# Kernel optimization log

Hardware: AMD Instinct MI355X
Metric: run time of the kernel (lower is better)

## Reference

```python
import jax, jax.numpy as jnp
import numpy as np

H, C = 8, 32          # heads, per-head channels (h_feats)
NEG_SLOPE = 0.2


def setup_inputs() -> dict:
    key = jax.random.key(0)
    ks = jax.random.split(key, 9)
    N, E, F_IN, F_E = 50000, 800000, 128, 16
    x = jax.random.normal(ks[0], (N, F_IN), jnp.float32)
    edge_index = jax.random.randint(ks[1], (2, E), 0, N, jnp.int64)
    edge_attr = jax.random.normal(ks[2], (E, F_E), jnp.float32)
    s = 1.0 / np.sqrt(F_IN)
    W = jax.random.normal(ks[3], (H * C, F_IN), jnp.float32) * s
    W_edge = jax.random.normal(ks[4], (H * C, F_E), jnp.float32) * (1.0 / np.sqrt(F_E))
    att_src = jax.random.normal(ks[5], (H, C), jnp.float32) * (1.0 / np.sqrt(C))
    att_dst = jax.random.normal(ks[6], (H, C), jnp.float32) * (1.0 / np.sqrt(C))
    att_edge = jax.random.normal(ks[7], (H, C), jnp.float32) * (1.0 / np.sqrt(C))
    bias = jnp.zeros((C,), jnp.float32)
    return {"x": x, "edge_index": edge_index, "edge_attr": edge_attr,
            "W": W, "W_edge": W_edge, "att_src": att_src, "att_dst": att_dst,
            "att_edge": att_edge, "bias": bias}


def reference(x, edge_index, edge_attr, W, W_edge, att_src, att_dst, att_edge, bias):
    N = x.shape[0]
    src, dst = edge_index[0], edge_index[1]

    # --- add self loops, edge_attr fill_value='mean' (per-dst mean of incoming attrs) ---
    deg = jax.ops.segment_sum(jnp.ones_like(dst, dtype=edge_attr.dtype), dst, num_segments=N)
    loop_attr = jax.ops.segment_sum(edge_attr, dst, num_segments=N) / jnp.maximum(deg, 1.0)[:, None]
    loop = jnp.arange(N, dtype=src.dtype)
    src = jnp.concatenate([src, loop])
    dst = jnp.concatenate([dst, loop])
    ea = jnp.concatenate([edge_attr, loop_attr], axis=0)  # [E+N, F_e]

    # --- node projection and per-node attention terms ---
    xh = (x @ W.T).reshape(N, H, C)                      # [N,H,C]
    a_src = jnp.einsum('nhc,hc->nh', xh, att_src)        # [N,H]
    a_dst = jnp.einsum('nhc,hc->nh', xh, att_dst)        # [N,H]

    # edge attention folded: (lin_edge(e).view(E,H,C) * att_edge).sum(-1) == e @ M
    M = jnp.einsum('hcf,hc->fh', W_edge.reshape(H, C, -1), att_edge)  # [F_e,H]
    a_edge = ea @ M                                      # [E+N,H]

    alpha = a_src[src] + a_dst[dst] + a_edge             # [E+N,H]
    alpha = jnp.where(alpha >= 0, alpha, NEG_SLOPE * alpha)

    # --- scatter-softmax over edges grouped by dst node ---
    amax = jax.ops.segment_max(alpha, dst, num_segments=N)  # every node has a self loop
    ex = jnp.exp(alpha - amax[dst])
    denom = jax.ops.segment_sum(ex, dst, num_segments=N)
    att = ex / denom[dst]                                # [E+N,H]

    # --- weighted message scatter-sum ---
    msg = xh[src] * att[..., None]                       # [E+N,H,C]
    out = jax.ops.segment_sum(msg, dst, num_segments=N)  # [N,H,C]
    return out.mean(axis=1) + bias                       # concat=False -> head mean
```

## Files before the change

kernel.cpp:

```cpp
#include <hip/hip_runtime.h>
#include <hip/hip_fp16.h>
#include <math.h>

#define H 8
#define C 32
#define HC 256
#define FE 16
#define FIN 128
#define NEG_SLOPE 0.2f

typedef __attribute__((ext_vector_type(8))) short bf16x8;
typedef __attribute__((ext_vector_type(4))) float f32x4;

__device__ __forceinline__ unsigned short f2bf(float f) {
  unsigned int u = __float_as_uint(f);
  unsigned int lsb = (u >> 16) & 1u;
  u += 0x7fffu + lsb;
  return (unsigned short)(u >> 16);
}
__device__ __forceinline__ float bf2f(unsigned short s) {
  return __uint_as_float(((unsigned int)s) << 16);
}
__device__ __forceinline__ unsigned short f2h(float f) {
  return __half_as_ushort(__float2half(f));
}
__device__ __forceinline__ float h2f(unsigned short s) {
  return __half2float(__ushort_as_half(s));
}

__device__ __forceinline__ void split8(const float* v, bf16x8& hi, bf16x8& lo) {
#pragma unroll
  for (int i = 0; i < 8; ++i) {
    unsigned int u = __float_as_uint(v[i]);
    unsigned int hu = u & 0xffff0000u;
    float r = v[i] - __uint_as_float(hu);
    hi[i] = (short)(hu >> 16);
    lo[i] = (short)f2bf(r);
  }
}

__global__ __launch_bounds__(256) void k_xh(const float* __restrict__ x,
                                            const unsigned short* __restrict__ Whi,
                                            const unsigned short* __restrict__ Wlo,
                                            const float* __restrict__ att_src,
                                            const float* __restrict__ att_dst,
                                            unsigned short* __restrict__ xhb,
                                            float* __restrict__ a_src,
                                            float* __restrict__ a_dst,
                                            unsigned short* __restrict__ a_srch, int N) {
  int t = threadIdx.x;
  int w = t >> 6, lane = t & 63;
  int n15 = lane & 15, q = lane >> 4;
  int nodeBase = blockIdx.x * 128 + w * 32;
  int chBase = blockIdx.y * 128;

  f32x4 acc[8][2];
#pragma unroll
  for (int mt = 0; mt < 8; ++mt)
#pragma unroll
    for (int nt = 0; nt < 2; ++nt) acc[mt][nt] = (f32x4)(0.f);

  for (int ks = 0; ks < 4; ++ks) {
    int kOff = ks * 32 + q * 8;
    bf16x8 Bhi[2], Blo[2];
#pragma unroll
    for (int nt = 0; nt < 2; ++nt) {
      int node = nodeBase + nt * 16 + n15;
      int rn = (node < N) ? node : (N - 1);
      const float* px = &x[(size_t)rn * FIN + kOff];
      float vb[8];
      *(float4*)&vb[0] = *(const float4*)px;
      *(float4*)&vb[4] = *(const float4*)(px + 4);
      split8(vb, Bhi[nt], Blo[nt]);
    }
#pragma unroll
    for (int mt = 0; mt < 8; ++mt) {
      int widx = ((chBase + mt * 16 + n15) << 7) + kOff;
      bf16x8 Ahi = *(const bf16x8*)&Whi[widx];
      bf16x8 Alo = *(const bf16x8*)&Wlo[widx];
#pragma unroll
      for (int nt = 0; nt < 2; ++nt) {
        acc[mt][nt] = __builtin_amdgcn_mfma_f32_16x16x32_bf16(Ahi, Bhi[nt], acc[mt][nt], 0, 0, 0);
        acc[mt][nt] = __builtin_amdgcn_mfma_f32_16x16x32_bf16(Ahi, Blo[nt], acc[mt][nt], 0, 0, 0);
        acc[mt][nt] = __builtin_amdgcn_mfma_f32_16x16x32_bf16(Alo, Bhi[nt], acc[mt][nt], 0, 0, 0);
      }
    }
  }

  float ps[2][4] = {{0.f,0.f,0.f,0.f},{0.f,0.f,0.f,0.f}};
  float pd[2][4] = {{0.f,0.f,0.f,0.f},{0.f,0.f,0.f,0.f}};
#pragma unroll
  for (int mt = 0; mt < 8; ++mt) {
    int hl = mt >> 1;
#pragma unroll
    for (int r = 0; r < 4; ++r) {
      int ch = chBase + mt * 16 + q * 4 + r;
      float as_c = att_src[ch], ad_c = att_dst[ch];
#pragma unroll
      for (int nt = 0; nt < 2; ++nt) {
        float val = acc[mt][nt][r];
        ps[nt][hl] = fmaf(val, as_c, ps[nt][hl]);
        pd[nt][hl] = fmaf(val, ad_c, pd[nt][hl]);
      }
    }
#pragma unroll
    for (int nt = 0; nt < 2; ++nt) {
      int node = nodeBase + nt * 16 + n15;
      if (node < N) {
        ushort4 us;
        us.x = f2bf(acc[mt][nt][0]); us.y = f2bf(acc[mt][nt][1]);
        us.z = f2bf(acc[mt][nt][2]); us.w = f2bf(acc[mt][nt][3]);
        *(ushort4*)&xhb[(size_t)node * HC + chBase + mt * 16 + q * 4] = us;
      }
    }
  }
#pragma unroll
  for (int nt = 0; nt < 2; ++nt)
#pragma unroll
    for (int hl = 0; hl < 4; ++hl) {
      ps[nt][hl] += __shfl_xor(ps[nt][hl], 16, 64);
      ps[nt][hl] += __shfl_xor(ps[nt][hl], 32, 64);
      pd[nt][hl] += __shfl_xor(pd[nt][hl], 16, 64);
      pd[nt][hl] += __shfl_xor(pd[nt][hl], 32, 64);
    }
  if (q == 0) {
#pragma unroll
    for (int nt = 0; nt < 2; ++nt) {
      int node = nodeBase + nt * 16 + n15;
      if (node < N) {
        *(float4*)&a_src[node * H + blockIdx.y * 4] = make_float4(ps[nt][0], ps[nt][1], ps[nt][2], ps[nt][3]);
        *(float4*)&a_dst[node * H + blockIdx.y * 4] = make_float4(pd[nt][0], pd[nt][1], pd[nt][2], pd[nt][3]);
        unsigned int p0 = (unsigned int)f2h(ps[nt][0]) | ((unsigned int)f2h(ps[nt][1]) << 16);
        unsigned int p1 = (unsigned int)f2h(ps[nt][2]) | ((unsigned int)f2h(ps[nt][3]) << 16);
        *(uint2*)&a_srch[(size_t)node * H + blockIdx.y * 4] = make_uint2(p0, p1);
      }
    }
  }
}

__global__ __launch_bounds__(256) void k_deg(const int* __restrict__ ei,
                                             int* __restrict__ deg,
                                             int* __restrict__ rank,
                                             const float* __restrict__ W,
                                             unsigned short* __restrict__ Whi,
                                             unsigned short* __restrict__ Wlo, int E) {
  int e = blockIdx.x * 256 + threadIdx.x;
  if (e < HC * FIN) {
    float v = W[e];
    unsigned int u = __float_as_uint(v);
    unsigned int hu = u & 0xffff0000u;
    Whi[e] = (unsigned short)(hu >> 16);
    Wlo[e] = f2bf(v - __uint_as_float(hu));
  }
  if (e < E) rank[e] = atomicAdd(&deg[ei[E + e]], 1);
}

__global__ __launch_bounds__(256) void k_scan1(const int* __restrict__ deg,
                                               int* __restrict__ bsum, int N) {
  int t = threadIdx.x;
  int i = blockIdx.x * 256 + t;
  int v = (i < N) ? deg[i] : 0;
#pragma unroll
  for (int m = 1; m < 64; m <<= 1) v += __shfl_xor(v, m, 64);
  __shared__ int wsum[4];
  if ((t & 63) == 0) wsum[t >> 6] = v;
  __syncthreads();
  if (t == 0) bsum[blockIdx.x] = wsum[0] + wsum[1] + wsum[2] + wsum[3];
}

__global__ __launch_bounds__(256) void k_scan23(const int* __restrict__ deg,
                                                const int* __restrict__ bsum,
                                                int* __restrict__ rowptr, int N, int E, int nb) {
  __shared__ int sb[256];
  __shared__ int buf[256];
  int t = threadIdx.x;
  sb[t] = (t < nb) ? bsum[t] : 0;
  int i = blockIdx.x * 256 + t;
  int v = (i < N) ? deg[i] : 0;
  buf[t] = v;
  __syncthreads();
  for (int off = 1; off < 256; off <<= 1) {
    int y1 = (t >= off) ? sb[t - off] : 0;
    int y2 = (t >= off) ? buf[t - off] : 0;
    __syncthreads();
    sb[t] += y1;
    buf[t] += y2;
    __syncthreads();
  }
  int bofs = (blockIdx.x == 0) ? 0 : sb[blockIdx.x - 1];
  if (i < N) rowptr[i] = bofs + buf[t] - v;
  if (i == 0) rowptr[N] = E;
}

__global__ __launch_bounds__(256) void k_edge_scatter(const int* __restrict__ ei,
                                                      const float* __restrict__ ea,
                                                      const float* __restrict__ W_edge,
                                                      const float* __restrict__ att_edge,
                                                      const unsigned short* __restrict__ a_srch,
                                                      const int* __restrict__ rowptr,
                                                      const int* __restrict__ rank,
                                                      unsigned int* __restrict__ recs,
                                                      int* __restrict__ sarr, int E) {
  __shared__ float Ms[FE * H];
  int t = threadIdx.x;
  if (t < FE * H) {
    int f = t >> 3, h = t & 7;
    float acc = 0.f;
#pragma unroll
    for (int c = 0; c < C; ++c)
      acc += W_edge[(h * C + c) * FE + f] * att_edge[h * C + c];
    Ms[f * H + h] = acc;
  }
  __syncthreads();
  int e0 = blockIdx.x * 512 + t;
  int e1 = e0 + 256;
  bool va = (e0 < E), vb = (e1 < E);
  int ca = va ? e0 : 0, cb = vb ? e1 : 0;
  int s0 = ei[ca], d0 = ei[E + ca];
  int s1 = ei[cb], d1 = ei[E + cb];
  const float4* pA = (const float4*)&ea[(size_t)ca * FE];
  const float4* pB = (const float4*)&ea[(size_t)cb * FE];
  float4 A0 = pA[0], A1 = pA[1], A2 = pA[2], A3 = pA[3];
  float4 B0 = pB[0], B1 = pB[1], B2 = pB[2], B3 = pB[3];
  int rk0 = rank[ca], rk1 = rank[cb];
  int rp0 = rowptr[d0], rp1 = rowptr[d1];
  uint4 asA = *(const uint4*)&a_srch[(size_t)s0 * H];
  uint4 asB = *(const uint4*)&a_srch[(size_t)s1 * H];

  float eavA[FE] = {A0.x, A0.y, A0.z, A0.w, A1.x, A1.y, A1.z, A1.w,
                    A2.x, A2.y, A2.z, A2.w, A3.x, A3.y, A3.z, A3.w};
  float eavB[FE] = {B0.x, B0.y, B0.z, B0.w, B1.x, B1.y, B1.z, B1.w,
                    B2.x, B2.y, B2.z, B2.w, B3.x, B3.y, B3.z, B3.w};
  float oA[H], oB[H];
#pragma unroll
  for (int h = 0; h < H; ++h) {
    float aa = 0.f, ab = 0.f;
#pragma unroll
    for (int f = 0; f < FE; ++f) {
      float m = Ms[f * H + h];
      aa += eavA[f] * m;
      ab += eavB[f] * m;
    }
    oA[h] = aa; oB[h] = ab;
  }
  unsigned int asw[2][4] = {{asA.x, asA.y, asA.z, asA.w}, {asB.x, asB.y, asB.z, asB.w}};
  if (va) {
    int pos = rp0 + rk0;
    unsigned int rec[H];
#pragma unroll
    for (int h = 0; h < H; ++h) {
      float asv = h2f((unsigned short)((h & 1) ? (asw[0][h >> 1] >> 16) : (asw[0][h >> 1] & 0xffffu)));
      rec[h] = (unsigned int)f2h(oA[h] + asv) | ((unsigned int)f2h(oA[h]) << 16);
    }
    uint4* rp = (uint4*)&recs[(size_t)pos * 8];
    rp[0] = make_uint4(rec[0], rec[1], rec[2], rec[3]);
    rp[1] = make_uint4(rec[4], rec[5], rec[6], rec[7]);
    sarr[pos] = s0;
  }
  if (vb) {
    int pos = rp1 + rk1;
    unsigned int rec[H];
#pragma unroll
    for (int h = 0; h < H; ++h) {
      float asv = h2f((unsigned short)((h & 1) ? (asw[1][h >> 1] >> 16) : (asw[1][h >> 1] & 0xffffu)));
      rec[h] = (unsigned int)f2h(oB[h] + asv) | ((unsigned int)f2h(oB[h]) << 16);
    }
    uint4* rp = (uint4*)&recs[(size_t)pos * 8];
    rp[0] = make_uint4(rec[0], rec[1], rec[2], rec[3]);
    rp[1] = make_uint4(rec[4], rec[5], rec[6], rec[7]);
    sarr[pos] = s1;
  }
}

__global__ __launch_bounds__(256) void k_node(const unsigned short* __restrict__ xhb,
                                              const float* __restrict__ a_src,
                                              const float* __restrict__ a_dst,
                                              const unsigned int* __restrict__ recs,
                                              const int* __restrict__ sarr,
                                              const int* __restrict__ rowptr,
                                              const float* __restrict__ bias,
                                              float* __restrict__ out, int N) {
  __shared__ float wlds[4][512];
  __shared__ int   slds[4][64];
  int wv = threadIdx.x >> 6;
  int lane = threadIdx.x & 63;
  int n = blockIdx.x * 4 + wv;
  if (n >= N) return;
  int start = rowptr[n];
  int deg = rowptr[n + 1] - start;
  int jmax = (deg < 64) ? deg : 64;
  int nit = (jmax + 7) >> 3;
  int padded = nit << 3;
  int h = lane & 7, esub = lane >> 3;
  float adst = a_dst[n * H + h];
  float asrc = a_src[n * H + h];

  if (lane < padded) slds[wv][lane] = (lane < jmax) ? sarr[start + lane] : n;

  const unsigned int* rb = recs + (size_t)start * 8 + lane;
  unsigned int u[8] = {0, 0, 0, 0, 0, 0, 0, 0};
#pragma unroll
  for (int it = 0; it < 8; ++it)
    if (it < nit) u[it] = rb[it * 64];

  float den = 0.f, psum = 0.f;
#pragma unroll
  for (int it = 0; it < 8; ++it)
    if (it < nit) {
      int j = it * 8 + esub;
      bool val = (j < jmax);
      float raw = h2f((unsigned short)(u[it] >> 16));
      float a = h2f((unsigned short)(u[it] & 0xffffu)) + adst;
      a = fmaxf(a, NEG_SLOPE * a);
      float w = val ? __expf(a) : 0.f;
      psum += val ? raw : 0.f;
      den += w;
      wlds[wv][it * 64 + lane] = w;
    }
  for (int j0 = 64; j0 < deg; j0 += 8) {
    int j = j0 + esub;
    if (j < deg) {
      unsigned int t = recs[(size_t)(start + j) * 8 + h];
      psum += h2f((unsigned short)(t >> 16));
      float a = h2f((unsigned short)(t & 0xffffu)) + adst;
      a = fmaxf(a, NEG_SLOPE * a);
      den += __expf(a);
    }
  }
#pragma unroll
  for (int m = 8; m <= 32; m <<= 1) {
    den += __shfl_xor(den, m, 64);
    psum += __shfl_xor(psum, m, 64);
  }
  float aself = asrc + adst + psum / fmaxf((float)deg, 1.f);
  aself = fmaxf(aself, NEG_SLOPE * aself);
  float wself = __expf(aself);
  float inv = 1.f / (den + wself);

  int hc = lane >> 3;
  float inv_c  = __shfl(inv, hc, 64);
  float ws_c   = __shfl(wself, hc, 64);
  float adst_c = __shfl(adst, hc, 64);
  float accx, accy, accz, accw;
  {
    uint2 su = ((const uint2*)(xhb + (((size_t)n) << 8)))[lane];
    accx = ws_c * __uint_as_float(su.x << 16);
    accy = ws_c * __uint_as_float(su.x & 0xffff0000u);
    accz = ws_c * __uint_as_float(su.y << 16);
    accw = ws_c * __uint_as_float(su.y & 0xffff0000u);
  }
  uint2 v0[8]; float w0[8];
  if (padded > 0) {
#pragma unroll
    for (int k = 0; k < 8; ++k) {
      w0[k] = wlds[wv][k * 8 + hc];
      v0[k] = ((const uint2*)(xhb + (((size_t)slds[wv][k]) << 8)))[lane];
    }
  }
  for (int j0 = 0; j0 < padded; j0 += 8) {
    uint2 v1[8]; float w1[8];
    int jn = j0 + 8;
    if (jn < padded) {
#pragma unroll
      for (int k = 0; k < 8; ++k) {
        w1[k] = wlds[wv][(jn + k) * 8 + hc];
        v1[k] = ((const uint2*)(xhb + (((size_t)slds[wv][jn + k]) << 8)))[lane];
      }
    }
#pragma unroll
    for (int k = 0; k < 8; ++k) {
      accx = fmaf(__uint_as_float(v0[k].x << 16), w0[k], accx);
      accy = fmaf(__uint_as_float(v0[k].x & 0xffff0000u), w0[k], accy);
      accz = fmaf(__uint_as_float(v0[k].y << 16), w0[k], accz);
      accw = fmaf(__uint_as_float(v0[k].y & 0xffff0000u), w0[k], accw);
    }
#pragma unroll
    for (int k = 0; k < 8; ++k) { v0[k] = v1[k]; w0[k] = w1[k]; }
  }
  for (int j = 64; j < deg; ++j) {
    unsigned int t = recs[(size_t)(start + j) * 8 + hc];
    int src = sarr[start + j];
    float a = h2f((unsigned short)(t & 0xffffu)) + adst_c;
    a = fmaxf(a, NEG_SLOPE * a);
    float wj = __expf(a);
    uint2 v = ((const uint2*)(xhb + (((size_t)src) << 8)))[lane];
    accx = fmaf(__uint_as_float(v.x << 16), wj, accx);
    accy = fmaf(__uint_as_float(v.x & 0xffff0000u), wj, accy);
    accz = fmaf(__uint_as_float(v.y << 16), wj, accz);
    accw = fmaf(__uint_as_float(v.y & 0xffff0000u), wj, accw);
  }
  accx *= inv_c; accy *= inv_c; accz *= inv_c; accw *= inv_c;

#pragma unroll
  for (int m = 8; m <= 32; m <<= 1) {
    accx += __shfl_xor(accx, m, 64);
    accy += __shfl_xor(accy, m, 64);
    accz += __shfl_xor(accz, m, 64);
    accw += __shfl_xor(accw, m, 64);
  }
  if (lane < 8) {
    float4 b = ((const float4*)bias)[lane];
    float4 o;
    o.x = accx * 0.125f + b.x;
    o.y = accy * 0.125f + b.y;
    o.z = accz * 0.125f + b.z;
    o.w = accw * 0.125f + b.w;
    ((float4*)&out[(size_t)n * C])[lane] = o;
  }
}

extern "C" void kernel_launch(void* const* d_in, const int* in_sizes, int n_in,
                              void* d_out, int out_size, void* d_ws, size_t ws_size,
                              hipStream_t stream) {
  const float* x        = (const float*)d_in[0];
  const int*   ei       = (const int*)d_in[1];
  const float* ea       = (const float*)d_in[2];
  const float* W        = (const float*)d_in[3];
  const float* W_edge   = (const float*)d_in[4];
  const float* att_src  = (const float*)d_in[5];
  const float* att_dst  = (const float*)d_in[6];
  const float* att_edge = (const float*)d_in[7];
  const float* bias     = (const float*)d_in[8];
  float* out = (float*)d_out;

  int N = in_sizes[0] / FIN;
  int E = in_sizes[1] / 2;
  int nb = (N + 255) / 256;

  char* ws = (char*)d_ws;
  auto take = [&](size_t bytes) {
    char* p = ws;
    ws += (bytes + 255) & ~(size_t)255;
    return p;
  };
  unsigned short* xhb    = (unsigned short*)take((size_t)N * HC * 2);
  float*          a_src  = (float*)take((size_t)N * H * 4);
  float*          a_dst  = (float*)take((size_t)N * H * 4);
  unsigned short* a_srch = (unsigned short*)take((size_t)N * H * 2);
  unsigned int*   recs   = (unsigned int*)take((size_t)E * 32);
  int*            sarr   = (int*)take((size_t)E * 4);
  unsigned short* Whi    = (unsigned short*)take((size_t)HC * FIN * 2);
  unsigned short* Wlo    = (unsigned short*)take((size_t)HC * FIN * 2);
  int*            deg    = (int*)take((size_t)N * 4);
  int*            rowptr = (int*)take((size_t)(N + 1) * 4);
  int*            rank   = (int*)take((size_t)E * 4);
  int*            bsum   = (int*)take((size_t)nb * 4);

  hipMemsetAsync(deg, 0, (size_t)N * 4, stream);
  k_deg<<<(E + 255) / 256, 256, 0, stream>>>(ei, deg, rank, W, Whi, Wlo, E);
  k_xh<<<dim3((N + 127) / 128, 2), 256, 0, stream>>>(x, Whi, Wlo, att_src, att_dst, xhb, a_src, a_dst, a_srch, N);
  k_scan1<<<nb, 256, 0, stream>>>(deg, bsum, N);
  k_scan23<<<nb, 256, 0, stream>>>(deg, bsum, rowptr, N, E, nb);
  k_edge_scatter<<<(E + 511) / 512, 256, 0, stream>>>(ei, ea, W_edge, att_edge, a_srch, rowptr, rank, recs, sarr, E);
  k_node<<<(N + 3) / 4, 256, 0, stream>>>(xhb, a_src, a_dst, recs, sarr, rowptr, bias, out, N);
}
```

Before: 303.4 us.

## Replace edge record scatter with permutation and compute edge attention in node kernel

The edge-scatter kernel, which computed per-edge attention logits and wrote 32-byte half-precision records plus source ids in CSR order, becomes a small kernel that writes only (src, edge id) pairs at each CSR position. The node kernel now gathers the edge attributes (64 bytes, in random original order), computes the edge attention term with the folded matrix held in shared memory, and adds the source term itself. This removes the record write and re-read but adds uncoalesced 64-byte gathers and extra math per edge in the node kernel. It also drops the software double buffering of the neighbour feature loads.

```diff
diff --git a/kernel.cpp b/kernel.cpp
--- a/kernel.cpp
+++ b/kernel.cpp
@@ -192,98 +192,49 @@
   if (i == 0) rowptr[N] = E;
 }
 
-__global__ __launch_bounds__(256) void k_edge_scatter(const int* __restrict__ ei,
-                                                      const float* __restrict__ ea,
-                                                      const float* __restrict__ W_edge,
-                                                      const float* __restrict__ att_edge,
-                                                      const unsigned short* __restrict__ a_srch,
-                                                      const int* __restrict__ rowptr,
-                                                      const int* __restrict__ rank,
-                                                      unsigned int* __restrict__ recs,
-                                                      int* __restrict__ sarr, int E) {
-  __shared__ float Ms[FE * H];
-  int t = threadIdx.x;
-  if (t < FE * H) {
-    int f = t >> 3, h = t & 7;
-    float acc = 0.f;
-#pragma unroll
-    for (int c = 0; c < C; ++c)
-      acc += W_edge[(h * C + c) * FE + f] * att_edge[h * C + c];
-    Ms[f * H + h] = acc;
-  }
-  __syncthreads();
-  int e0 = blockIdx.x * 512 + t;
+__global__ __launch_bounds__(256) void k_perm(const int* __restrict__ ei,
+                                              const int* __restrict__ rowptr,
+                                              const int* __restrict__ rank,
+                                              int2* __restrict__ pr, int E) {
+  int e0 = blockIdx.x * 512 + threadIdx.x;
   int e1 = e0 + 256;
   bool va = (e0 < E), vb = (e1 < E);
   int ca = va ? e0 : 0, cb = vb ? e1 : 0;
   int s0 = ei[ca], d0 = ei[E + ca];
   int s1 = ei[cb], d1 = ei[E + cb];
-  const float4* pA = (const float4*)&ea[(size_t)ca * FE];
-  const float4* pB = (const float4*)&ea[(size_t)cb * FE];
-  float4 A0 = pA[0], A1 = pA[1], A2 = pA[2], A3 = pA[3];
-  float4 B0 = pB[0], B1 = pB[1], B2 = pB[2], B3 = pB[3];
   int rk0 = rank[ca], rk1 = rank[cb];
   int rp0 = rowptr[d0], rp1 = rowptr[d1];
-  uint4 asA = *(const uint4*)&a_srch[(size_t)s0 * H];
-  uint4 asB = *(const uint4*)&a_srch[(size_t)s1 * H];
-
-  float eavA[FE] = {A0.x, A0.y, A0.z, A0.w, A1.x, A1.y, A1.z, A1.w,
-                    A2.x, A2.y, A2.z, A2.w, A3.x, A3.y, A3.z, A3.w};
-  float eavB[FE] = {B0.x, B0.y, B0.z, B0.w, B1.x, B1.y, B1.z, B1.w,
-                    B2.x, B2.y, B2.z, B2.w, B3.x, B3.y, B3.z, B3.w};
-  float oA[H], oB[H];
-#pragma unroll
-  for (int h = 0; h < H; ++h) {
-    float aa = 0.f, ab = 0.f;
-#pragma unroll
-    for (int f = 0; f < FE; ++f) {
-      float m = Ms[f * H + h];
-      aa += eavA[f] * m;
-      ab += eavB[f] * m;
-    }
-    oA[h] = aa; oB[h] = ab;
-  }
-  unsigned int asw[2][4] = {{asA.x, asA.y, asA.z, asA.w}, {asB.x, asB.y, asB.z, asB.w}};
-  if (va) {
-    int pos = rp0 + rk0;
-    unsigned int rec[H];
-#pragma unroll
-    for (int h = 0; h < H; ++h) {
-      float asv = h2f((unsigned short)((h & 1) ? (asw[0][h >> 1] >> 16) : (asw[0][h >> 1] & 0xffffu)));
-      rec[h] = (unsigned int)f2h(oA[h] + asv) | ((unsigned int)f2h(oA[h]) << 16);
-    }
-    uint4* rp = (uint4*)&recs[(size_t)pos * 8];
-    rp[0] = make_uint4(rec[0], rec[1], rec[2], rec[3]);
-    rp[1] = make_uint4(rec[4], rec[5], rec[6], rec[7]);
-    sarr[pos] = s0;
-  }
-  if (vb) {
-    int pos = rp1 + rk1;
-    unsigned int rec[H];
-#pragma unroll
-    for (int h = 0; h < H; ++h) {
-      float asv = h2f((unsigned short)((h & 1) ? (asw[1][h >> 1] >> 16) : (asw[1][h >> 1] & 0xffffu)));
-      rec[h] = (unsigned int)f2h(oB[h] + asv) | ((unsigned int)f2h(oB[h]) << 16);
-    }
-    uint4* rp = (uint4*)&recs[(size_t)pos * 8];
-    rp[0] = make_uint4(rec[0], rec[1], rec[2], rec[3]);
-    rp[1] = make_uint4(rec[4], rec[5], rec[6], rec[7]);
-    sarr[pos] = s1;
-  }
+  if (va) pr[rp0 + rk0] = make_int2(s0, ca);
+  if (vb) pr[rp1 + rk1] = make_int2(s1, cb);
 }
 
 __global__ __launch_bounds__(256) void k_node(const unsigned short* __restrict__ xhb,
                                               const float* __restrict__ a_src,
+                                              const unsigned short* __restrict__ a_srch,
                                               const float* __restrict__ a_dst,
-                                              const unsigned int* __restrict__ recs,
-                                              const int* __restrict__ sarr,
+                                              const float* __restrict__ ea,
+                                              const float* __restrict__ W_edge,
+                                              const float* __restrict__ att_edge,
+                                              const int2* __restrict__ pr,
                                               const int* __restrict__ rowptr,
                                               const float* __restrict__ bias,
                                               float* __restrict__ out, int N) {
+  __shared__ float Ms[FE * H];
   __shared__ float wlds[4][512];
   __shared__ int   slds[4][64];
-  int wv = threadIdx.x >> 6;
-  int lane = threadIdx.x & 63;
+  int t = threadIdx.x;
+  if (t < FE * H) {
+    int f = t >> 3, hh = t & 7;
+    float acc = 0.f;
+#pragma unroll
+    for (int c = 0; c < C; ++c)
+      acc += W_edge[(hh * C + c) * FE + f] * att_edge[hh * C + c];
+    Ms[f * H + hh] = acc;
+  }
+  __syncthreads();
+
+  int wv = t >> 6;
+  int lane = t & 63;
   int n = blockIdx.x * 4 + wv;
   if (n >= N) return;
   int start = rowptr[n];
@@ -295,13 +246,20 @@
   float adst = a_dst[n * H + h];
   float asrc = a_src[n * H + h];
 
-  if (lane < padded) slds[wv][lane] = (lane < jmax) ? sarr[start + lane] : n;
-
-  const unsigned int* rb = recs + (size_t)start * 8 + lane;
-  unsigned int u[8] = {0, 0, 0, 0, 0, 0, 0, 0};
-#pragma unroll
-  for (int it = 0; it < 8; ++it)
-    if (it < nit) u[it] = rb[it * 64];
+  int2 pe[8];
+#pragma unroll
+  for (int it = 0; it < 8; ++it) {
+    pe[it] = make_int2(n, 0);
+    if (it < nit) {
+      int j = it * 8 + esub;
+      if (j < jmax) pe[it] = pr[start + j];
+    }
+  }
+  if (h == 0) {
+#pragma unroll
+    for (int it = 0; it < 8; ++it)
+      if (it < nit) slds[wv][it * 8 + esub] = pe[it].x;
+  }
 
   float den = 0.f, psum = 0.f;
 #pragma unroll
@@ -309,21 +267,36 @@
     if (it < nit) {
       int j = it * 8 + esub;
       bool val = (j < jmax);
-      float raw = h2f((unsigned short)(u[it] >> 16));
-      float a = h2f((unsigned short)(u[it] & 0xffffu)) + adst;
+      const float4* pq = (const float4*)&ea[(size_t)pe[it].y * FE];
+      float4 q0 = pq[0], q1 = pq[1], q2 = pq[2], q3 = pq[3];
+      float ev[16] = {q0.x, q0.y, q0.z, q0.w, q1.x, q1.y, q1.z, q1.w,
+                      q2.x, q2.y, q2.z, q2.w, q3.x, q3.y, q3.z, q3.w};
+      float aev = 0.f;
+#pragma unroll
+      for (int f = 0; f < FE; ++f) aev = fmaf(ev[f], Ms[f * H + h], aev);
+      float asv = h2f(a_srch[(size_t)pe[it].x * H + h]);
+      float a = aev + asv + adst;
       a = fmaxf(a, NEG_SLOPE * a);
       float w = val ? __expf(a) : 0.f;
-      psum += val ? raw : 0.f;
+      psum += val ? aev : 0.f;
       den += w;
       wlds[wv][it * 64 + lane] = w;
     }
   for (int j0 = 64; j0 < deg; j0 += 8) {
     int j = j0 + esub;
     if (j < deg) {
-      unsigned int t = recs[(size_t)(start + j) * 8 + h];
-      psum += h2f((unsigned short)(t >> 16));
-      float a = h2f((unsigned short)(t & 0xffffu)) + adst;
+      int2 pe2 = pr[start + j];
+      const float4* pq = (const float4*)&ea[(size_t)pe2.y * FE];
+      float4 q0 = pq[0], q1 = pq[1], q2 = pq[2], q3 = pq[3];
+      float ev[16] = {q0.x, q0.y, q0.z, q0.w, q1.x, q1.y, q1.z, q1.w,
+                      q2.x, q2.y, q2.z, q2.w, q3.x, q3.y, q3.z, q3.w};
+      float aev = 0.f;
+#pragma unroll
+      for (int f = 0; f < FE; ++f) aev = fmaf(ev[f], Ms[f * H + h], aev);
+      float asv = h2f(a_srch[(size_t)pe2.x * H + h]);
+      float a = aev + asv + adst;
       a = fmaxf(a, NEG_SLOPE * a);
+      psum += aev;
       den += __expf(a);
     }
   }
@@ -349,41 +322,35 @@
     accz = ws_c * __uint_as_float(su.y << 16);
     accw = ws_c * __uint_as_float(su.y & 0xffff0000u);
   }
-  uint2 v0[8]; float w0[8];
-  if (padded > 0) {
+  for (int j0 = 0; j0 < padded; j0 += 8) {
+    uint2 v[8]; float wj[8];
 #pragma unroll
     for (int k = 0; k < 8; ++k) {
-      w0[k] = wlds[wv][k * 8 + hc];
-      v0[k] = ((const uint2*)(xhb + (((size_t)slds[wv][k]) << 8)))[lane];
-    }
-  }
-  for (int j0 = 0; j0 < padded; j0 += 8) {
-    uint2 v1[8]; float w1[8];
-    int jn = j0 + 8;
-    if (jn < padded) {
-#pragma unroll
-      for (int k = 0; k < 8; ++k) {
-        w1[k] = wlds[wv][(jn + k) * 8 + hc];
-        v1[k] = ((const uint2*)(xhb + (((size_t)slds[wv][jn + k]) << 8)))[lane];
-      }
+      wj[k] = wlds[wv][(j0 + k) * 8 + hc];
+      v[k] = ((const uint2*)(xhb + (((size_t)slds[wv][j0 + k]) << 8)))[lane];
     }
 #pragma unroll
     for (int k = 0; k < 8; ++k) {
-      accx = fmaf(__uint_as_float(v0[k].x << 16), w0[k], accx);
-      accy = fmaf(__uint_as_float(v0[k].x & 0xffff0000u), w0[k], accy);
-      accz = fmaf(__uint_as_float(v0[k].y << 16), w0[k], accz);
-      accw = fmaf(__uint_as_float(v0[k].y & 0xffff0000u), w0[k], accw);
-    }
-#pragma unroll
-    for (int k = 0; k < 8; ++k) { v0[k] = v1[k]; w0[k] = w1[k]; }
+      accx = fmaf(__uint_as_float(v[k].x << 16), wj[k], accx);
+      accy = fmaf(__uint_as_float(v[k].x & 0xffff0000u), wj[k], accy);
+      accz = fmaf(__uint_as_float(v[k].y << 16), wj[k], accz);
+      accw = fmaf(__uint_as_float(v[k].y & 0xffff0000u), wj[k], accw);
+    }
   }
   for (int j = 64; j < deg; ++j) {
-    unsigned int t = recs[(size_t)(start + j) * 8 + hc];
-    int src = sarr[start + j];
-    float a = h2f((unsigned short)(t & 0xffffu)) + adst_c;
+    int2 pe2 = pr[start + j];
+    const float4* pq = (const float4*)&ea[(size_t)pe2.y * FE];
+    float4 q0 = pq[0], q1 = pq[1], q2 = pq[2], q3 = pq[3];
+    float ev[16] = {q0.x, q0.y, q0.z, q0.w, q1.x, q1.y, q1.z, q1.w,
+                    q2.x, q2.y, q2.z, q2.w, q3.x, q3.y, q3.z, q3.w};
+    float aev = 0.f;
+#pragma unroll
+    for (int f = 0; f < FE; ++f) aev = fmaf(ev[f], Ms[f * H + hc], aev);
+    float asv = h2f(a_srch[(size_t)pe2.x * H + hc]);
+    float a = aev + asv + adst_c;
     a = fmaxf(a, NEG_SLOPE * a);
     float wj = __expf(a);
-    uint2 v = ((const uint2*)(xhb + (((size_t)src) << 8)))[lane];
+    uint2 v = ((const uint2*)(xhb + (((size_t)pe2.x) << 8)))[lane];
     accx = fmaf(__uint_as_float(v.x << 16), wj, accx);
     accy = fmaf(__uint_as_float(v.x & 0xffff0000u), wj, accy);
     accz = fmaf(__uint_as_float(v.y << 16), wj, accz);
@@ -437,8 +404,7 @@
   float*          a_src  = (float*)take((size_t)N * H * 4);
   float*          a_dst  = (float*)take((size_t)N * H * 4);
   unsigned short* a_srch = (unsigned short*)take((size_t)N * H * 2);
-  unsigned int*   recs   = (unsigned int*)take((size_t)E * 32);
-  int*            sarr   = (int*)take((size_t)E * 4);
+  int2*           pr     = (int2*)take((size_t)E * 8);
   unsigned short* Whi    = (unsigned short*)take((size_t)HC * FIN * 2);
   unsigned short* Wlo    = (unsigned short*)take((size_t)HC * FIN * 2);
   int*            deg    = (int*)take((size_t)N * 4);
@@ -451,6 +417,6 @@
   k_xh<<<dim3((N + 127) / 128, 2), 256, 0, stream>>>(x, Whi, Wlo, att_src, att_dst, xhb, a_src, a_dst, a_srch, N);
   k_scan1<<<nb, 256, 0, stream>>>(deg, bsum, N);
   k_scan23<<<nb, 256, 0, stream>>>(deg, bsum, rowptr, N, E, nb);
-  k_edge_scatter<<<(E + 511) / 512, 256, 0, stream>>>(ei, ea, W_edge, att_edge, a_srch, rowptr, rank, recs, sarr, E);
-  k_node<<<(N + 3) / 4, 256, 0, stream>>>(xhb, a_src, a_dst, recs, sarr, rowptr, bias, out, N);
-}
+  k_perm<<<(E + 511) / 512, 256, 0, stream>>>(ei, rowptr, rank, pr, E);
+  k_node<<<(N + 3) / 4, 256, 0, stream>>>(xhb, a_src, a_srch, a_dst, ea, W_edge, att_edge, pr, rowptr, bias, out, N);
+}
```

New measurement: 335.7 us. 1.11x slower.

## Halve edge records, atomically accumulate self-loop edge sums, drop fp32 a_src

Applied to the files above, without the earlier changes.

Edge records shrink from 32 to 16 bytes per edge by storing only the fp16 pre-activation logit. The raw edge-attention term needed for the self-loop mean is accumulated into a per-destination buffer with float atomics in the scatter kernel. The node kernel reads the fp16 a_src copy instead of a separate fp32 array, and the software double-buffer in the gather loop is replaced by a simple per-chunk load loop. This cuts write and read traffic on the edge arrays, at the cost of 8 atomics per edge and possibly less latency hiding in the gather.

```diff
diff --git a/kernel.cpp b/kernel.cpp
--- a/kernel.cpp
+++ b/kernel.cpp
@@ -45,7 +45,6 @@
                                             const float* __restrict__ att_src,
                                             const float* __restrict__ att_dst,
                                             unsigned short* __restrict__ xhb,
-                                            float* __restrict__ a_src,
                                             float* __restrict__ a_dst,
                                             unsigned short* __restrict__ a_srch, int N) {
   int t = threadIdx.x;
@@ -128,7 +127,6 @@
     for (int nt = 0; nt < 2; ++nt) {
       int node = nodeBase + nt * 16 + n15;
       if (node < N) {
-        *(float4*)&a_src[node * H + blockIdx.y * 4] = make_float4(ps[nt][0], ps[nt][1], ps[nt][2], ps[nt][3]);
         *(float4*)&a_dst[node * H + blockIdx.y * 4] = make_float4(pd[nt][0], pd[nt][1], pd[nt][2], pd[nt][3]);
         unsigned int p0 = (unsigned int)f2h(ps[nt][0]) | ((unsigned int)f2h(ps[nt][1]) << 16);
         unsigned int p1 = (unsigned int)f2h(ps[nt][2]) | ((unsigned int)f2h(ps[nt][3]) << 16);
@@ -199,8 +197,9 @@
                                                       const unsigned short* __restrict__ a_srch,
                                                       const int* __restrict__ rowptr,
                                                       const int* __restrict__ rank,
-                                                      unsigned int* __restrict__ recs,
-                                                      int* __restrict__ sarr, int E) {
+                                                      unsigned short* __restrict__ recs16,
+                                                      int* __restrict__ sarr,
+                                                      float* __restrict__ aesum, int E) {
   __shared__ float Ms[FE * H];
   int t = threadIdx.x;
   if (t < FE * H) {
@@ -246,38 +245,43 @@
   unsigned int asw[2][4] = {{asA.x, asA.y, asA.z, asA.w}, {asB.x, asB.y, asB.z, asB.w}};
   if (va) {
     int pos = rp0 + rk0;
-    unsigned int rec[H];
-#pragma unroll
-    for (int h = 0; h < H; ++h) {
-      float asv = h2f((unsigned short)((h & 1) ? (asw[0][h >> 1] >> 16) : (asw[0][h >> 1] & 0xffffu)));
-      rec[h] = (unsigned int)f2h(oA[h] + asv) | ((unsigned int)f2h(oA[h]) << 16);
-    }
-    uint4* rp = (uint4*)&recs[(size_t)pos * 8];
-    rp[0] = make_uint4(rec[0], rec[1], rec[2], rec[3]);
-    rp[1] = make_uint4(rec[4], rec[5], rec[6], rec[7]);
+    unsigned int r01 = 0, r23 = 0, r45 = 0, r67 = 0;
+    unsigned int rw[4];
+#pragma unroll
+    for (int p = 0; p < 4; ++p) {
+      float as_lo = h2f((unsigned short)(asw[0][p] & 0xffffu));
+      float as_hi = h2f((unsigned short)(asw[0][p] >> 16));
+      rw[p] = (unsigned int)f2h(oA[2 * p] + as_lo) | ((unsigned int)f2h(oA[2 * p + 1] + as_hi) << 16);
+    }
+    r01 = rw[0]; r23 = rw[1]; r45 = rw[2]; r67 = rw[3];
+    *(uint4*)&recs16[(size_t)pos * 8] = make_uint4(r01, r23, r45, r67);
     sarr[pos] = s0;
+#pragma unroll
+    for (int h = 0; h < H; ++h) atomicAdd(&aesum[(size_t)d0 * H + h], oA[h]);
   }
   if (vb) {
     int pos = rp1 + rk1;
-    unsigned int rec[H];
-#pragma unroll
-    for (int h = 0; h < H; ++h) {
-      float asv = h2f((unsigned short)((h & 1) ? (asw[1][h >> 1] >> 16) : (asw[1][h >> 1] & 0xffffu)));
-      rec[h] = (unsigned int)f2h(oB[h] + asv) | ((unsigned int)f2h(oB[h]) << 16);
-    }
-    uint4* rp = (uint4*)&recs[(size_t)pos * 8];
-    rp[0] = make_uint4(rec[0], rec[1], rec[2], rec[3]);
-    rp[1] = make_uint4(rec[4], rec[5], rec[6], rec[7]);
+    unsigned int rw[4];
+#pragma unroll
+    for (int p = 0; p < 4; ++p) {
+      float as_lo = h2f((unsigned short)(asw[1][p] & 0xffffu));
+      float as_hi = h2f((unsigned short)(asw[1][p] >> 16));
+      rw[p] = (unsigned int)f2h(oB[2 * p] + as_lo) | ((unsigned int)f2h(oB[2 * p + 1] + as_hi) << 16);
+    }
+    *(uint4*)&recs16[(size_t)pos * 8] = make_uint4(rw[0], rw[1], rw[2], rw[3]);
     sarr[pos] = s1;
+#pragma unroll
+    for (int h = 0; h < H; ++h) atomicAdd(&aesum[(size_t)d1 * H + h], oB[h]);
   }
 }
 
 __global__ __launch_bounds__(256) void k_node(const unsigned short* __restrict__ xhb,
-                                              const float* __restrict__ a_src,
+                                              const unsigned short* __restrict__ a_srch,
                                               const float* __restrict__ a_dst,
-                                              const unsigned int* __restrict__ recs,
+                                              const unsigned short* __restrict__ recs16,
                                               const int* __restrict__ sarr,
                                               const int* __restrict__ rowptr,
+                                              const float* __restrict__ aesum,
                                               const float* __restrict__ bias,
                                               float* __restrict__ out, int N) {
   __shared__ float wlds[4][512];
@@ -293,46 +297,44 @@
   int padded = nit << 3;
   int h = lane & 7, esub = lane >> 3;
   float adst = a_dst[n * H + h];
-  float asrc = a_src[n * H + h];
+  float asrc = h2f(a_srch[(size_t)n * H + h]);
+  float aes  = aesum[(size_t)n * H + h];
 
   if (lane < padded) slds[wv][lane] = (lane < jmax) ? sarr[start + lane] : n;
 
-  const unsigned int* rb = recs + (size_t)start * 8 + lane;
-  unsigned int u[8] = {0, 0, 0, 0, 0, 0, 0, 0};
-#pragma unroll
-  for (int it = 0; it < 8; ++it)
-    if (it < nit) u[it] = rb[it * 64];
-
-  float den = 0.f, psum = 0.f;
+  const unsigned short* rb = recs16 + (size_t)start * 8 + lane;
+  unsigned short u[8];
+#pragma unroll
+  for (int it = 0; it < 8; ++it) {
+    u[it] = 0;
+    if (it < nit) {
+      int j = it * 8 + esub;
+      if (j < jmax) u[it] = rb[it * 64];
+    }
+  }
+
+  float den = 0.f;
 #pragma unroll
   for (int it = 0; it < 8; ++it)
     if (it < nit) {
       int j = it * 8 + esub;
-      bool val = (j < jmax);
-      float raw = h2f((unsigned short)(u[it] >> 16));
-      float a = h2f((unsigned short)(u[it] & 0xffffu)) + adst;
+      float a = h2f(u[it]) + adst;
       a = fmaxf(a, NEG_SLOPE * a);
-      float w = val ? __expf(a) : 0.f;
-      psum += val ? raw : 0.f;
+      float w = (j < jmax) ? __expf(a) : 0.f;
       den += w;
       wlds[wv][it * 64 + lane] = w;
     }
   for (int j0 = 64; j0 < deg; j0 += 8) {
     int j = j0 + esub;
     if (j < deg) {
-      unsigned int t = recs[(size_t)(start + j) * 8 + h];
-      psum += h2f((unsigned short)(t >> 16));
-      float a = h2f((unsigned short)(t & 0xffffu)) + adst;
+      float a = h2f(recs16[(size_t)(start + j) * 8 + h]) + adst;
       a = fmaxf(a, NEG_SLOPE * a);
       den += __expf(a);
     }
   }
 #pragma unroll
-  for (int m = 8; m <= 32; m <<= 1) {
-    den += __shfl_xor(den, m, 64);
-    psum += __shfl_xor(psum, m, 64);
-  }
-  float aself = asrc + adst + psum / fmaxf((float)deg, 1.f);
+  for (int m = 8; m <= 32; m <<= 1) den += __shfl_xor(den, m, 64);
+  float aself = asrc + adst + aes / fmaxf((float)deg, 1.f);
   aself = fmaxf(aself, NEG_SLOPE * aself);
   float wself = __expf(aself);
   float inv = 1.f / (den + wself);
@@ -349,38 +351,24 @@
     accz = ws_c * __uint_as_float(su.y << 16);
     accw = ws_c * __uint_as_float(su.y & 0xffff0000u);
   }
-  uint2 v0[8]; float w0[8];
-  if (padded > 0) {
+  for (int j0 = 0; j0 < padded; j0 += 8) {
+    uint2 v[8]; float wj[8];
 #pragma unroll
     for (int k = 0; k < 8; ++k) {
-      w0[k] = wlds[wv][k * 8 + hc];
-      v0[k] = ((const uint2*)(xhb + (((size_t)slds[wv][k]) << 8)))[lane];
-    }
-  }
-  for (int j0 = 0; j0 < padded; j0 += 8) {
-    uint2 v1[8]; float w1[8];
-    int jn = j0 + 8;
-    if (jn < padded) {
-#pragma unroll
-      for (int k = 0; k < 8; ++k) {
-        w1[k] = wlds[wv][(jn + k) * 8 + hc];
-        v1[k] = ((const uint2*)(xhb + (((size_t)slds[wv][jn + k]) << 8)))[lane];
-      }
+      wj[k] = wlds[wv][(j0 + k) * 8 + hc];
+      v[k] = ((const uint2*)(xhb + (((size_t)slds[wv][j0 + k]) << 8)))[lane];
     }
 #pragma unroll
     for (int k = 0; k < 8; ++k) {
-      accx = fmaf(__uint_as_float(v0[k].x << 16), w0[k], accx);
-      accy = fmaf(__uint_as_float(v0[k].x & 0xffff0000u), w0[k], accy);
-      accz = fmaf(__uint_as_float(v0[k].y << 16), w0[k], accz);
-      accw = fmaf(__uint_as_float(v0[k].y & 0xffff0000u), w0[k], accw);
-    }
-#pragma unroll
-    for (int k = 0; k < 8; ++k) { v0[k] = v1[k]; w0[k] = w1[k]; }
+      accx = fmaf(__uint_as_float(v[k].x << 16), wj[k], accx);
+      accy = fmaf(__uint_as_float(v[k].x & 0xffff0000u), wj[k], accy);
+      accz = fmaf(__uint_as_float(v[k].y << 16), wj[k], accz);
+      accw = fmaf(__uint_as_float(v[k].y & 0xffff0000u), wj[k], accw);
+    }
   }
   for (int j = 64; j < deg; ++j) {
-    unsigned int t = recs[(size_t)(start + j) * 8 + hc];
     int src = sarr[start + j];
-    float a = h2f((unsigned short)(t & 0xffffu)) + adst_c;
+    float a = h2f(recs16[(size_t)(start + j) * 8 + hc]) + adst_c;
     a = fmaxf(a, NEG_SLOPE * a);
     float wj = __expf(a);
     uint2 v = ((const uint2*)(xhb + (((size_t)src) << 8)))[lane];
@@ -434,23 +422,23 @@
     return p;
   };
   unsigned short* xhb    = (unsigned short*)take((size_t)N * HC * 2);
-  float*          a_src  = (float*)take((size_t)N * H * 4);
   float*          a_dst  = (float*)take((size_t)N * H * 4);
   unsigned short* a_srch = (unsigned short*)take((size_t)N * H * 2);
-  unsigned int*   recs   = (unsigned int*)take((size_t)E * 32);
+  unsigned short* recs16 = (unsigned short*)take((size_t)E * 16);
   int*            sarr   = (int*)take((size_t)E * 4);
   unsigned short* Whi    = (unsigned short*)take((size_t)HC * FIN * 2);
   unsigned short* Wlo    = (unsigned short*)take((size_t)HC * FIN * 2);
-  int*            deg    = (int*)take((size_t)N * 4);
+  int*            deg    = (int*)take((size_t)N * 4 + (size_t)N * H * 4);
+  float*          aesum  = (float*)(deg + N);
   int*            rowptr = (int*)take((size_t)(N + 1) * 4);
   int*            rank   = (int*)take((size_t)E * 4);
   int*            bsum   = (int*)take((size_t)nb * 4);
 
-  hipMemsetAsync(deg, 0, (size_t)N * 4, stream);
+  hipMemsetAsync(deg, 0, (size_t)N * 4 + (size_t)N * H * 4, stream);
   k_deg<<<(E + 255) / 256, 256, 0, stream>>>(ei, deg, rank, W, Whi, Wlo, E);
-  k_xh<<<dim3((N + 127) / 128, 2), 256, 0, stream>>>(x, Whi, Wlo, att_src, att_dst, xhb, a_src, a_dst, a_srch, N);
+  k_xh<<<dim3((N + 127) / 128, 2), 256, 0, stream>>>(x, Whi, Wlo, att_src, att_dst, xhb, a_dst, a_srch, N);
   k_scan1<<<nb, 256, 0, stream>>>(deg, bsum, N);
   k_scan23<<<nb, 256, 0, stream>>>(deg, bsum, rowptr, N, E, nb);
-  k_edge_scatter<<<(E + 511) / 512, 256, 0, stream>>>(ei, ea, W_edge, att_edge, a_srch, rowptr, rank, recs, sarr, E);
-  k_node<<<(N + 3) / 4, 256, 0, stream>>>(xhb, a_src, a_dst, recs, sarr, rowptr, bias, out, N);
-}
+  k_edge_scatter<<<(E + 511) / 512, 256, 0, stream>>>(ei, ea, W_edge, att_edge, a_srch, rowptr, rank, recs16, sarr, aesum, E);
+  k_node<<<(N + 3) / 4, 256, 0, stream>>>(xhb, a_srch, a_dst, recs16, sarr, rowptr, aesum, bias, out, N);
+}
```

Result: slower. 591.5 us (+94.9%).
